# Kernel optimization log

Hardware: AMD Instinct MI355X
Metric: run time of the kernel (lower is better)

## Reference

```python
import jax, jax.numpy as jnp
import numpy as np

# Sizes from init_kwargs / input_specs
D_MODEL = 1024; D_INT = 64; KW = 32; B = 2; L = 4096
SAMPLING = np.array([5, 5, 2, 1, 1]); DILATIONS = np.array([1, 1, 2, 4, 8])
SUBHEADS = len(SAMPLING); HEADS = int(SAMPLING.sum())  # 5, 14
HEAD_OF_SUB = np.repeat(np.arange(SUBHEADS), SAMPLING)  # subhead index for each head
HEAD_DIL = np.repeat(DILATIONS, SAMPLING)                # dilation for each head


def _win_idx(dil):
    # centered dilated band, clipped at sequence edges -> [L, KW]
    offs = (np.arange(KW) - KW // 2) * dil
    return np.clip(np.arange(L)[:, None] + offs[None, :], 0, L - 1)

SUB_IDX = jnp.asarray(np.stack([_win_idx(d) for d in DILATIONS]))  # [SUBHEADS, L, KW]
HEAD_IDX = jnp.asarray(np.stack([_win_idx(d) for d in HEAD_DIL]))  # [HEADS, L, KW]


def setup_inputs() -> dict:
    rng = jax.random.key(0)
    ks = jax.random.split(rng, 9)
    n = lambda i, sh, sc=1.0: jax.random.normal(ks[i], sh, dtype=jnp.float32) * sc
    return dict(
        query=n(0, (B, L, D_MODEL)),
        key=n(1, (B, L, D_MODEL)),
        value=n(2, (B, L, D_MODEL)),
        Wq=n(3, (SUBHEADS, D_MODEL, D_INT), 0.02),
        bq=jnp.zeros((SUBHEADS, D_INT), jnp.float32),
        Wk=n(4, (SUBHEADS, D_MODEL, D_INT), 0.02),
        bk=jnp.zeros((SUBHEADS, D_INT), jnp.float32),
        Wv=n(5, (HEADS, D_MODEL, D_INT), 0.02),
        bv=jnp.zeros((HEADS, D_INT), jnp.float32),
        Ws=n(6, (HEADS, KW, KW), 0.05) + jnp.eye(KW, dtype=jnp.float32)[None],
        bs=jnp.zeros((HEADS, KW), jnp.float32),
        Wc=n(7, (HEADS * D_INT, D_MODEL), 0.02),
        bc=jnp.zeros((D_MODEL,), jnp.float32),
    )


def reference(query, key, value, Wq, bq, Wk, bk, Wv, bv, Ws, bs, Wc, bc):
    # per-subhead query/key projections: [S, B, L, Di]
    q = jnp.einsum('bld,sdi->sbli', query, Wq) + bq[:, None, None, :]
    k = jnp.einsum('bld,sdi->sbli', key, Wk) + bk[:, None, None, :]
    # per-head value projection: [H, B, L, Di]
    v = jnp.einsum('bld,hdi->hbli', value, Wv) + bv[:, None, None, :]
    # dilated banded key windows per subhead: [S, B, L, KW, Di]
    kw = jax.vmap(lambda kh, ix: kh[:, ix], in_axes=(0, 0))(k, SUB_IDX)
    # banded scores [S, B, L, KW]
    scores = jnp.einsum('sbli,sblki->sblk', q, kw) / jnp.sqrt(jnp.float32(D_INT))
    # supersample: replicate each subhead's scores to its heads -> [H, B, L, KW]
    scores_h = scores[HEAD_OF_SUB]
    # per-head positional supersampling linear on the score window
    sampled = jnp.einsum('hblk,hkm->hblm', scores_h, Ws) + bs[:, None, None, :]
    attn = jax.nn.softmax(sampled, axis=-1)
    # dilated value windows per head: [H, B, L, KW, Di]
    vw = jax.vmap(lambda vh, ix: vh[:, ix], in_axes=(0, 0))(v, HEAD_IDX)
    out = jnp.einsum('hblk,hblki->hbli', attn, vw)  # [H, B, L, Di]
    out = jnp.transpose(out, (1, 2, 0, 3)).reshape(B, L, HEADS * D_INT)
    return out @ Wc + bc  # [B, L, D_MODEL]
```

## Files before the change

### kernel.cpp

```cpp
#include <hip/hip_runtime.h>
#include <math.h>

#define D_MODEL 1024
#define D_INT   64
#define KW      32
#define L_SEQ   4096
#define SUBHEADS 5
#define HEADS   14
#define M_ROWS  8192
#define N_CAT   896
#define NQK     320

typedef unsigned short us;
typedef unsigned int   uu;
typedef __attribute__((ext_vector_type(4))) unsigned int uu4;
typedef __attribute__((ext_vector_type(8))) short bf16x8_t;
typedef __attribute__((ext_vector_type(4))) float f32x4_t;

__device__ __forceinline__ float u2f(uu u) {
    float f; __builtin_memcpy(&f, &u, 4); return f;
}
__device__ __forceinline__ float blo(uu u) { return u2f(u << 16); }
__device__ __forceinline__ float bhi(uu u) { return u2f(u & 0xffff0000u); }
__device__ __forceinline__ us f2b(float f) {
    uu u; __builtin_memcpy(&u, &f, 4);
    u += 0x7fffu + ((u >> 16) & 1u);
    return (us)(u >> 16);
}
__device__ __forceinline__ uu pack2(float a, float b) {
    return (uu)f2b(a) | ((uu)f2b(b) << 16);
}
__device__ __forceinline__ uu cvtpk(float a, float b) {
    uu r;
    asm("v_cvt_pk_bf16_f32 %0, %1, %2" : "=v"(r) : "v"(a), "v"(b));
    return r;
}
__device__ __forceinline__ void load16(void* lds, const void* g) {
    __builtin_amdgcn_global_load_lds(
        (const __attribute__((address_space(1))) unsigned int*)g,
        (__attribute__((address_space(3))) unsigned int*)lds, 16, 0, 0);
}
__device__ __forceinline__ int dil_of_sub(int s) {
    return (s <= 1) ? 1 : (1 << (s - 1));
}
__device__ __forceinline__ int hstart_of_sub(int s) {
    return (s == 0) ? 0 : (s == 1) ? 5 : (s == 2) ? 10 : (s == 3) ? 12 : 13;
}
__device__ __forceinline__ int hcount_of_sub(int s) {
    return (s <= 1) ? 5 : (s == 2) ? 2 : 1;
}

#define CAST_BLK 1536
__global__ __launch_bounds__(256)
void prep_kernel(const float4* __restrict__ q, const float4* __restrict__ k,
                 const float4* __restrict__ v,
                 const float* __restrict__ Wq, const float* __restrict__ Wk,
                 const float* __restrict__ Wv, const float* __restrict__ Wc,
                 us* __restrict__ Xq, us* __restrict__ Xk, us* __restrict__ Xv,
                 us* __restrict__ Wqt, us* __restrict__ Wkt,
                 us* __restrict__ Wvt, us* __restrict__ Wct)
{
    __shared__ float t[32][33];
    const int tid = threadIdx.x;
    const int b = blockIdx.x;

    if (b < CAST_BLK) {
        const int arr = b >> 9;
        const int blk = b & 511;
        const float4* s = (arr == 0) ? q : (arr == 1) ? k : v;
        uu4* d = (uu4*)((arr == 0) ? Xq : (arr == 1) ? Xk : Xv);
        const int tg = blk * 256 + tid;
#pragma unroll
        for (int it = 0; it < 8; it++) {
            const int i = tg + it * 131072;
            float4 x0 = s[2 * i];
            float4 x1 = s[2 * i + 1];
            uu4 o;
            o.x = cvtpk(x0.x, x0.y); o.y = cvtpk(x0.z, x0.w);
            o.z = cvtpk(x1.x, x1.y); o.w = cvtpk(x1.z, x1.w);
            d[i] = o;
        }
        return;
    }

    int g = b - CAST_BLK;
    const float* S; us* D; int K, N;
    if (g < 640) {
        if (g < 320) { S = Wq; D = Wqt; } else { S = Wk; D = Wkt; g -= 320; }
        K = 1024; N = 64;
    } else if (g < 1536) {
        g -= 640; S = Wv; D = Wvt; K = 1024; N = 64;
    } else {
        g -= 1536; S = Wc; D = Wct; K = 896; N = 1024;
    }
    const int nkx = K >> 5;
    const int kx = g % nkx;
    const int rest = g / nkx;
    const int ny = rest % (N >> 5);
    const int z  = rest / (N >> 5);
    const int k0 = kx * 32, n0 = ny * 32;
    S += (size_t)z * K * N;
    D += (size_t)z * K * N;
    const int tx = tid & 31, ty = tid >> 5;
#pragma unroll
    for (int r = 0; r < 32; r += 8)
        t[r + ty][tx] = S[(size_t)(k0 + r + ty) * N + n0 + tx];
    __syncthreads();
#pragma unroll
    for (int r = 0; r < 32; r += 8)
        D[(size_t)(n0 + r + ty) * K + k0 + tx] = f2b(t[tx][r + ty]);
}

__device__ __forceinline__
void gemm64_core(const us* __restrict__ A, const us* __restrict__ Bt,
                 const float* __restrict__ bias, us* __restrict__ C,
                 int K, int ldC, int row0, int col0, us* As, us* Bs)
{
    const int tid = threadIdx.x, w = tid >> 6, lane = tid & 63;
    const int m = lane & 15, quad = lane >> 4;
    const int sr = lane >> 3;
    const int scs = (lane & 7) ^ sr;

    f32x4_t z4 = {0.f, 0.f, 0.f, 0.f};
    f32x4_t acc[2][4] = {{z4, z4, z4, z4}, {z4, z4, z4, z4}};

    for (int k0 = 0; k0 < K; k0 += 64) {
#pragma unroll
        for (int p = 0; p < 4; p++) {
            const int r = w * 32 + p * 8 + sr;
            load16(&As[(w * 32 + p * 8) * 64], A + (size_t)(row0 + r) * K + k0 + scs * 8);
        }
#pragma unroll
        for (int p = 0; p < 2; p++) {
            const int r = w * 16 + p * 8 + sr;
            load16(&Bs[(w * 16 + p * 8) * 64], Bt + (size_t)(col0 + r) * K + k0 + scs * 8);
        }
        __syncthreads();
#pragma unroll
        for (int ks = 0; ks < 2; ks++) {
            const int slot = ((ks * 4 + quad) ^ (m & 7)) * 8;
            bf16x8_t a0 = *(const bf16x8_t*)&As[(w * 32 + m) * 64 + slot];
            bf16x8_t a1 = *(const bf16x8_t*)&As[(w * 32 + 16 + m) * 64 + slot];
#pragma unroll
            for (int t = 0; t < 4; t++) {
                bf16x8_t bb = *(const bf16x8_t*)&Bs[(t * 16 + m) * 64 + slot];
                acc[0][t] = __builtin_amdgcn_mfma_f32_16x16x32_bf16(a0, bb, acc[0][t], 0, 0, 0);
                acc[1][t] = __builtin_amdgcn_mfma_f32_16x16x32_bf16(a1, bb, acc[1][t], 0, 0, 0);
            }
        }
        __syncthreads();
    }

#pragma unroll
    for (int tm = 0; tm < 2; tm++) {
        const int rbase = row0 + w * 32 + tm * 16 + quad * 4;
#pragma unroll
        for (int t = 0; t < 4; t++) {
            const int col = col0 + t * 16 + m;
            const float bi = bias[col];
#pragma unroll
            for (int r = 0; r < 4; r++)
                C[(size_t)(rbase + r) * ldC + col] = f2b(acc[tm][t][r] + bi);
        }
    }
}

__device__ __forceinline__
void gemm128_core(const us* __restrict__ A, const us* __restrict__ Bt,
                  const float* __restrict__ bias, void* __restrict__ Cv,
                  int K, int ldC, int outBf16, int row0, int col0,
                  us* As, us* Bs)
{
    const int tid = threadIdx.x, w = tid >> 6, lane = tid & 63;
    const int m = lane & 15, quad = lane >> 4;
    const int sr = lane >> 3;
    const int scs = (lane & 7) ^ sr;
    const int mrow0 = (w & 1) * 64, ncol0 = (w >> 1) * 64;

    f32x4_t z = {0.f, 0.f, 0.f, 0.f};
    f32x4_t acc[4][4] = {{z,z,z,z},{z,z,z,z},{z,z,z,z},{z,z,z,z}};

    for (int k0 = 0; k0 < K; k0 += 64) {
#pragma unroll
        for (int p = 0; p < 4; p++) {
            const int r = w * 32 + p * 8 + sr;
            load16(&As[(w * 32 + p * 8) * 64], A  + (size_t)(row0 + r) * K + k0 + scs * 8);
            load16(&Bs[(w * 32 + p * 8) * 64], Bt + (size_t)(col0 + r) * K + k0 + scs * 8);
        }
        __syncthreads();
#pragma unroll
        for (int ks = 0; ks < 2; ks++) {
            const int slot = ((ks * 4 + quad) ^ (m & 7)) * 8;
            bf16x8_t a[4], b[4];
#pragma unroll
            for (int t = 0; t < 4; t++) {
                a[t] = *(const bf16x8_t*)&As[(mrow0 + t * 16 + m) * 64 + slot];
                b[t] = *(const bf16x8_t*)&Bs[(ncol0 + t * 16 + m) * 64 + slot];
            }
#pragma unroll
            for (int i = 0; i < 4; i++)
#pragma unroll
                for (int j = 0; j < 4; j++)
                    acc[i][j] = __builtin_amdgcn_mfma_f32_16x16x32_bf16(a[i], b[j], acc[i][j], 0, 0, 0);
        }
        __syncthreads();
    }

#pragma unroll
    for (int i = 0; i < 4; i++) {
        const int rbase = row0 + mrow0 + i * 16 + quad * 4;
        if (outBf16) {
            us* Cb = (us*)Cv;
#pragma unroll
            for (int j = 0; j < 4; j++) {
                const int col = col0 + ncol0 + j * 16 + m;
                const float bi = bias[col];
#pragma unroll
                for (int r = 0; r < 4; r++)
                    Cb[(size_t)(rbase + r) * ldC + col] = f2b(acc[i][j][r] + bi);
            }
        } else {
            float* Cb = (float*)Cv;
#pragma unroll
            for (int j = 0; j < 4; j++) {
                const int col = col0 + ncol0 + j * 16 + m;
                const float bi = bias[col];
#pragma unroll
                for (int r = 0; r < 4; r++)
                    Cb[(size_t)(rbase + r) * ldC + col] = acc[i][j][r] + bi;
            }
        }
    }
}

__global__ __launch_bounds__(256)
void proj_kernel(const us* __restrict__ Xq, const us* __restrict__ Xk,
                 const us* __restrict__ Xv,
                 const us* __restrict__ Wqt, const us* __restrict__ Wkt,
                 const us* __restrict__ Wvt,
                 const float* __restrict__ bq, const float* __restrict__ bk,
                 const float* __restrict__ bv,
                 us* __restrict__ qbuf, us* __restrict__ kbuf,
                 us* __restrict__ vbuf)
{
    __shared__ us As[128 * 64];
    __shared__ us Bs[128 * 64];
    const int b = blockIdx.x;
    if (b < 448) {
        const int bx = b & 63, cy = b >> 6;
        gemm128_core(Xv, Wvt, bv, vbuf, D_MODEL, N_CAT, 1,
                     bx << 7, cy << 7, As, Bs);
    } else {
        const int idx = b - 448;
        const int bx = idx & 63;
        const int rest = idx >> 6;
        const int cy = rest % 5, z = rest / 5;
        gemm64_core(z ? Xk : Xq, z ? Wkt : Wqt, z ? bk : bq,
                    z ? kbuf : qbuf, D_MODEL, NQK,
                    bx << 7, cy << 6, As, Bs);
    }
}

__global__ __launch_bounds__(256)
void gemm_out(const us* __restrict__ ab, const us* __restrict__ Wct,
              const float* __restrict__ bc, float* __restrict__ out)
{
    __shared__ us As[128 * 64];
    __shared__ us Bs[128 * 64];
    gemm128_core(ab, Wct, bc, out, N_CAT, D_MODEL, 0,
                 (int)(blockIdx.x << 7), (int)(blockIdx.y << 7), As, Bs);
}

template<int ROWS>
__global__ __launch_bounds__(256)
void attn_kernel(const us* __restrict__ qb, const us* __restrict__ kb,
                 const us* __restrict__ vb,
                 const float* __restrict__ Ws, const float* __restrict__ bs,
                 us* __restrict__ ab, int sbase)
{
    __shared__ uu    kq[ROWS * 36 + 64 * 32];
    __shared__ float sab[64 * 36];
    __shared__ float atn[64 * 36];

    uu* kslab = kq;
    uu* qslab = kq + ROWS * 36;
    uu* vslab = kq;

    const int tid  = threadIdx.x;
    const int wave = tid >> 6;
    const int lane = tid & 63;
    const int j    = lane & 31;
    const int half = lane >> 5;
    const int s    = sbase + blockIdx.y;
    const int d    = dil_of_sub(s);
    const int ml0  = blockIdx.x * 64;
    const int l0   = ml0 & 4095;
    const int bm   = ml0 - l0;
    const int W    = 64 + 31 * d;

    const uu4* kg4 = (const uu4*)kb;
    const uu4* qg4 = (const uu4*)qb;
    for (int idx = tid; idx < W * 8; idx += 256) {
        int r = idx >> 3, c4 = idx & 7;
        int src = l0 - 16 * d + r;
        src = src < 0 ? 0 : (src > 4095 ? 4095 : src);
        *(uu4*)&kslab[r * 36 + c4 * 4] = kg4[(size_t)(bm + src) * 40 + s * 8 + c4];
    }
    for (int idx = tid; idx < 64 * 8; idx += 256) {
        int r = idx >> 3, c4 = idx & 7;
        *(uu4*)&qslab[r * 32 + c4 * 4] = qg4[(size_t)(ml0 + r) * 40 + s * 8 + c4];
    }
    __syncthreads();

#pragma unroll
    for (int i = 0; i < 8; i++) {
        const int p = wave * 16 + i * 2 + half;
        const uu4* k4 = (const uu4*)&kslab[(p + j * d) * 36];
        const uu4* q4 = (const uu4*)&qslab[p * 32];
        float acc = 0.f;
#pragma unroll
        for (int q = 0; q < 8; q++) {
            uu4 kd = k4[q];
            uu4 qd = q4[q];
            acc = fmaf(blo(kd.x), blo(qd.x), acc); acc = fmaf(bhi(kd.x), bhi(qd.x), acc);
            acc = fmaf(blo(kd.y), blo(qd.y), acc); acc = fmaf(bhi(kd.y), bhi(qd.y), acc);
            acc = fmaf(blo(kd.z), blo(qd.z), acc); acc = fmaf(bhi(kd.z), bhi(qd.z), acc);
            acc = fmaf(blo(kd.w), blo(qd.w), acc); acc = fmaf(bhi(kd.w), bhi(qd.w), acc);
        }
        sab[p * 36 + j] = acc * 0.125f;
    }
    __syncthreads();

    const int h0 = hstart_of_sub(s);
    const int hc = hcount_of_sub(s);
    const uu4* vg4 = (const uu4*)vb;

    for (int hh = h0; hh < h0 + hc; hh++) {
        for (int idx = tid; idx < W * 8; idx += 256) {
            int r = idx >> 3, c4 = idx & 7;
            int src = l0 - 16 * d + r;
            src = src < 0 ? 0 : (src > 4095 ? 4095 : src);
            *(uu4*)&vslab[r * 36 + c4 * 4] = vg4[(size_t)(bm + src) * 112 + hh * 8 + c4];
        }
        float wsr[32];
#pragma unroll
        for (int k = 0; k < 32; k++) wsr[k] = Ws[(size_t)hh * 1024 + k * 32 + j];
        const float bsv = bs[hh * 32 + j];

#pragma unroll
        for (int i = 0; i < 8; i++) {
            const int p = wave * 16 + i * 2 + half;
            const float4* s4 = (const float4*)&sab[p * 36];
            float acc = bsv;
#pragma unroll
            for (int q = 0; q < 8; q++) {
                float4 v = s4[q];
                acc = fmaf(v.x, wsr[q * 4 + 0], acc);
                acc = fmaf(v.y, wsr[q * 4 + 1], acc);
                acc = fmaf(v.z, wsr[q * 4 + 2], acc);
                acc = fmaf(v.w, wsr[q * 4 + 3], acc);
            }
            float mx = acc;
#pragma unroll
            for (int off = 16; off > 0; off >>= 1) mx = fmaxf(mx, __shfl_xor(mx, off, 64));
            float ex = __expf(acc - mx);
            float sum = ex;
#pragma unroll
            for (int off = 16; off > 0; off >>= 1) sum += __shfl_xor(sum, off, 64);
            atn[p * 36 + j] = ex / sum;
        }
        __syncthreads();

        const int o = lane >> 3;
        const int c = lane & 7;
#pragma unroll
        for (int pass = 0; pass < 2; pass++) {
            const int p  = wave * 16 + pass * 8 + o;
            const int ml = ml0 + p;
            float a0 = 0.f, a1 = 0.f, a2 = 0.f, a3 = 0.f;
            float a4 = 0.f, a5 = 0.f, a6 = 0.f, a7 = 0.f;
#pragma unroll
            for (int mm = 0; mm < 32; mm++) {
                const float at = atn[p * 36 + mm];
                uu4 vd = *(const uu4*)&vslab[(p + mm * d) * 36 + c * 4];
                a0 = fmaf(blo(vd.x), at, a0); a1 = fmaf(bhi(vd.x), at, a1);
                a2 = fmaf(blo(vd.y), at, a2); a3 = fmaf(bhi(vd.y), at, a3);
                a4 = fmaf(blo(vd.z), at, a4); a5 = fmaf(bhi(vd.z), at, a5);
                a6 = fmaf(blo(vd.w), at, a6); a7 = fmaf(bhi(vd.w), at, a7);
            }
            uu4 od;
            od.x = pack2(a0, a1); od.y = pack2(a2, a3);
            od.z = pack2(a4, a5); od.w = pack2(a6, a7);
            *(uu4*)&((uu*)ab)[(size_t)ml * 448 + hh * 32 + c * 4] = od;
        }
        __syncthreads();
    }
}

extern "C" void kernel_launch(void* const* d_in, const int* in_sizes, int n_in,
                              void* d_out, int out_size, void* d_ws, size_t ws_size,
                              hipStream_t stream)
{
    const float* query = (const float*)d_in[0];
    const float* key   = (const float*)d_in[1];
    const float* value = (const float*)d_in[2];
    const float* Wq    = (const float*)d_in[3];
    const float* bq    = (const float*)d_in[4];
    const float* Wk    = (const float*)d_in[5];
    const float* bk    = (const float*)d_in[6];
    const float* Wv    = (const float*)d_in[7];
    const float* bv    = (const float*)d_in[8];
    const float* Ws    = (const float*)d_in[9];
    const float* bs    = (const float*)d_in[10];
    const float* Wc    = (const float*)d_in[11];
    const float* bc    = (const float*)d_in[12];
    float* out = (float*)d_out;

    us* w = (us*)d_ws;
    us* Xq  = w;
    us* ab  = w;
    us* Xk  = Xq  + (size_t)M_ROWS * D_MODEL;
    us* Xv  = Xk  + (size_t)M_ROWS * D_MODEL;
    us* Wqt = Xv  + (size_t)M_ROWS * D_MODEL;
    us* Wkt = Wqt + (size_t)SUBHEADS * D_INT * D_MODEL;
    us* Wvt = Wkt + (size_t)SUBHEADS * D_INT * D_MODEL;
    us* Wct = Wvt + (size_t)HEADS * D_INT * D_MODEL;
    us* qbuf = Wct + (size_t)D_MODEL * N_CAT;
    us* kbuf = qbuf + (size_t)M_ROWS * NQK;
    us* vbuf = kbuf + (size_t)M_ROWS * NQK;

    dim3 blk(256);

    prep_kernel<<<dim3(CAST_BLK + 2432), blk, 0, stream>>>(
        (const float4*)query, (const float4*)key, (const float4*)value,
        Wq, Wk, Wv, Wc, Xq, Xk, Xv, Wqt, Wkt, Wvt, Wct);

    proj_kernel<<<dim3(1088), blk, 0, stream>>>(
        Xq, Xk, Xv, Wqt, Wkt, Wvt, bq, bk, bv, qbuf, kbuf, vbuf);

    attn_kernel<95><<<dim3(M_ROWS / 64, 2), blk, 0, stream>>>(
        qbuf, kbuf, vbuf, Ws, bs, ab, 0);
    attn_kernel<312><<<dim3(M_ROWS / 64, 3), blk, 0, stream>>>(
        qbuf, kbuf, vbuf, Ws, bs, ab, 2);

    gemm_out<<<dim3(M_ROWS / 128, D_MODEL / 128), blk, 0, stream>>>(
        ab, Wct, bc, out);
}
```

Measured before the change: 304.3 us.

## Parallelize attention over heads instead of subheads, recomputing shared scores per head

The attention kernels now launch one block per (row tile, head) instead of one per (row tile, subhead) looping over that subhead's heads. Each block recomputes the banded QK scores for its subhead, then does the supersampling, softmax and value aggregation for a single head, reusing the score buffer for the attention weights and the K slab for V. This raises grid parallelism and cuts the serialized per-head loop and its syncs, at the cost of redundant QK score computation and K loads for heads sharing a subhead.

New measurement: 284.5 us. 6.5% less time.

```diff
diff --git a/kernel.cpp b/kernel.cpp
--- a/kernel.cpp
+++ b/kernel.cpp
@@ -40,14 +40,11 @@
         (const __attribute__((address_space(1))) unsigned int*)g,
         (__attribute__((address_space(3))) unsigned int*)lds, 16, 0, 0);
 }
+__device__ __forceinline__ int subhead_of(int h) {
+    return (h < 5) ? 0 : (h < 10) ? 1 : (h < 12) ? 2 : (h == 12) ? 3 : 4;
+}
 __device__ __forceinline__ int dil_of_sub(int s) {
     return (s <= 1) ? 1 : (1 << (s - 1));
-}
-__device__ __forceinline__ int hstart_of_sub(int s) {
-    return (s == 0) ? 0 : (s == 1) ? 5 : (s == 2) ? 10 : (s == 3) ? 12 : 13;
-}
-__device__ __forceinline__ int hcount_of_sub(int s) {
-    return (s <= 1) ? 5 : (s == 2) ? 2 : 1;
 }
 
 #define CAST_BLK 1536
@@ -276,22 +273,19 @@
 void attn_kernel(const us* __restrict__ qb, const us* __restrict__ kb,
                  const us* __restrict__ vb,
                  const float* __restrict__ Ws, const float* __restrict__ bs,
-                 us* __restrict__ ab, int sbase)
-{
-    __shared__ uu    kq[ROWS * 36 + 64 * 32];
+                 us* __restrict__ ab, int hbase)
+{
+    __shared__ uu    kv[ROWS * 36];
+    __shared__ uu    qslab[64 * 32];
     __shared__ float sab[64 * 36];
-    __shared__ float atn[64 * 36];
-
-    uu* kslab = kq;
-    uu* qslab = kq + ROWS * 36;
-    uu* vslab = kq;
 
     const int tid  = threadIdx.x;
     const int wave = tid >> 6;
     const int lane = tid & 63;
     const int j    = lane & 31;
     const int half = lane >> 5;
-    const int s    = sbase + blockIdx.y;
+    const int h    = hbase + blockIdx.y;
+    const int s    = subhead_of(h);
     const int d    = dil_of_sub(s);
     const int ml0  = blockIdx.x * 64;
     const int l0   = ml0 & 4095;
@@ -304,7 +298,7 @@
         int r = idx >> 3, c4 = idx & 7;
         int src = l0 - 16 * d + r;
         src = src < 0 ? 0 : (src > 4095 ? 4095 : src);
-        *(uu4*)&kslab[r * 36 + c4 * 4] = kg4[(size_t)(bm + src) * 40 + s * 8 + c4];
+        *(uu4*)&kv[r * 36 + c4 * 4] = kg4[(size_t)(bm + src) * 40 + s * 8 + c4];
     }
     for (int idx = tid; idx < 64 * 8; idx += 256) {
         int r = idx >> 3, c4 = idx & 7;
@@ -315,7 +309,7 @@
 #pragma unroll
     for (int i = 0; i < 8; i++) {
         const int p = wave * 16 + i * 2 + half;
-        const uu4* k4 = (const uu4*)&kslab[(p + j * d) * 36];
+        const uu4* k4 = (const uu4*)&kv[(p + j * d) * 36];
         const uu4* q4 = (const uu4*)&qslab[p * 32];
         float acc = 0.f;
 #pragma unroll
@@ -331,69 +325,63 @@
     }
     __syncthreads();
 
-    const int h0 = hstart_of_sub(s);
-    const int hc = hcount_of_sub(s);
     const uu4* vg4 = (const uu4*)vb;
-
-    for (int hh = h0; hh < h0 + hc; hh++) {
-        for (int idx = tid; idx < W * 8; idx += 256) {
-            int r = idx >> 3, c4 = idx & 7;
-            int src = l0 - 16 * d + r;
-            src = src < 0 ? 0 : (src > 4095 ? 4095 : src);
-            *(uu4*)&vslab[r * 36 + c4 * 4] = vg4[(size_t)(bm + src) * 112 + hh * 8 + c4];
-        }
-        float wsr[32];
-#pragma unroll
-        for (int k = 0; k < 32; k++) wsr[k] = Ws[(size_t)hh * 1024 + k * 32 + j];
-        const float bsv = bs[hh * 32 + j];
-
-#pragma unroll
-        for (int i = 0; i < 8; i++) {
-            const int p = wave * 16 + i * 2 + half;
-            const float4* s4 = (const float4*)&sab[p * 36];
-            float acc = bsv;
-#pragma unroll
-            for (int q = 0; q < 8; q++) {
-                float4 v = s4[q];
-                acc = fmaf(v.x, wsr[q * 4 + 0], acc);
-                acc = fmaf(v.y, wsr[q * 4 + 1], acc);
-                acc = fmaf(v.z, wsr[q * 4 + 2], acc);
-                acc = fmaf(v.w, wsr[q * 4 + 3], acc);
-            }
-            float mx = acc;
-#pragma unroll
-            for (int off = 16; off > 0; off >>= 1) mx = fmaxf(mx, __shfl_xor(mx, off, 64));
-            float ex = __expf(acc - mx);
-            float sum = ex;
-#pragma unroll
-            for (int off = 16; off > 0; off >>= 1) sum += __shfl_xor(sum, off, 64);
-            atn[p * 36 + j] = ex / sum;
-        }
-        __syncthreads();
-
-        const int o = lane >> 3;
-        const int c = lane & 7;
-#pragma unroll
-        for (int pass = 0; pass < 2; pass++) {
-            const int p  = wave * 16 + pass * 8 + o;
-            const int ml = ml0 + p;
-            float a0 = 0.f, a1 = 0.f, a2 = 0.f, a3 = 0.f;
-            float a4 = 0.f, a5 = 0.f, a6 = 0.f, a7 = 0.f;
-#pragma unroll
-            for (int mm = 0; mm < 32; mm++) {
-                const float at = atn[p * 36 + mm];
-                uu4 vd = *(const uu4*)&vslab[(p + mm * d) * 36 + c * 4];
-                a0 = fmaf(blo(vd.x), at, a0); a1 = fmaf(bhi(vd.x), at, a1);
-                a2 = fmaf(blo(vd.y), at, a2); a3 = fmaf(bhi(vd.y), at, a3);
-                a4 = fmaf(blo(vd.z), at, a4); a5 = fmaf(bhi(vd.z), at, a5);
-                a6 = fmaf(blo(vd.w), at, a6); a7 = fmaf(bhi(vd.w), at, a7);
-            }
-            uu4 od;
-            od.x = pack2(a0, a1); od.y = pack2(a2, a3);
-            od.z = pack2(a4, a5); od.w = pack2(a6, a7);
-            *(uu4*)&((uu*)ab)[(size_t)ml * 448 + hh * 32 + c * 4] = od;
-        }
-        __syncthreads();
+    for (int idx = tid; idx < W * 8; idx += 256) {
+        int r = idx >> 3, c4 = idx & 7;
+        int src = l0 - 16 * d + r;
+        src = src < 0 ? 0 : (src > 4095 ? 4095 : src);
+        *(uu4*)&kv[r * 36 + c4 * 4] = vg4[(size_t)(bm + src) * 112 + h * 8 + c4];
+    }
+    float wsr[32];
+#pragma unroll
+    for (int k = 0; k < 32; k++) wsr[k] = Ws[(size_t)h * 1024 + k * 32 + j];
+    const float bsv = bs[h * 32 + j];
+
+#pragma unroll
+    for (int i = 0; i < 8; i++) {
+        const int p = wave * 16 + i * 2 + half;
+        const float4* s4 = (const float4*)&sab[p * 36];
+        float acc = bsv;
+#pragma unroll
+        for (int q = 0; q < 8; q++) {
+            float4 v = s4[q];
+            acc = fmaf(v.x, wsr[q * 4 + 0], acc);
+            acc = fmaf(v.y, wsr[q * 4 + 1], acc);
+            acc = fmaf(v.z, wsr[q * 4 + 2], acc);
+            acc = fmaf(v.w, wsr[q * 4 + 3], acc);
+        }
+        float mx = acc;
+#pragma unroll
+        for (int off = 16; off > 0; off >>= 1) mx = fmaxf(mx, __shfl_xor(mx, off, 64));
+        float ex = __expf(acc - mx);
+        float sum = ex;
+#pragma unroll
+        for (int off = 16; off > 0; off >>= 1) sum += __shfl_xor(sum, off, 64);
+        sab[p * 36 + j] = ex / sum;
+    }
+    __syncthreads();
+
+    const int o = lane >> 3;
+    const int c = lane & 7;
+#pragma unroll
+    for (int pass = 0; pass < 2; pass++) {
+        const int p  = wave * 16 + pass * 8 + o;
+        const int ml = ml0 + p;
+        float a0 = 0.f, a1 = 0.f, a2 = 0.f, a3 = 0.f;
+        float a4 = 0.f, a5 = 0.f, a6 = 0.f, a7 = 0.f;
+#pragma unroll
+        for (int mm = 0; mm < 32; mm++) {
+            const float at = sab[p * 36 + mm];
+            uu4 vd = *(const uu4*)&kv[(p + mm * d) * 36 + c * 4];
+            a0 = fmaf(blo(vd.x), at, a0); a1 = fmaf(bhi(vd.x), at, a1);
+            a2 = fmaf(blo(vd.y), at, a2); a3 = fmaf(bhi(vd.y), at, a3);
+            a4 = fmaf(blo(vd.z), at, a4); a5 = fmaf(bhi(vd.z), at, a5);
+            a6 = fmaf(blo(vd.w), at, a6); a7 = fmaf(bhi(vd.w), at, a7);
+        }
+        uu4 od;
+        od.x = pack2(a0, a1); od.y = pack2(a2, a3);
+        od.z = pack2(a4, a5); od.w = pack2(a6, a7);
+        *(uu4*)&((uu*)ab)[(size_t)ml * 448 + h * 32 + c * 4] = od;
     }
 }
 
@@ -438,10 +426,10 @@
     proj_kernel<<<dim3(1088), blk, 0, stream>>>(
         Xq, Xk, Xv, Wqt, Wkt, Wvt, bq, bk, bv, qbuf, kbuf, vbuf);
 
-    attn_kernel<95><<<dim3(M_ROWS / 64, 2), blk, 0, stream>>>(
+    attn_kernel<95><<<dim3(M_ROWS / 64, 10), blk, 0, stream>>>(
         qbuf, kbuf, vbuf, Ws, bs, ab, 0);
-    attn_kernel<312><<<dim3(M_ROWS / 64, 3), blk, 0, stream>>>(
-        qbuf, kbuf, vbuf, Ws, bs, ab, 2);
+    attn_kernel<312><<<dim3(M_ROWS / 64, 4), blk, 0, stream>>>(
+        qbuf, kbuf, vbuf, Ws, bs, ab, 10);
 
     gemm_out<<<dim3(M_ROWS / 128, D_MODEL / 128), blk, 0, stream>>>(
         ab, Wct, bc, out);
```
